# Performance work log

Hardware: AMD Instinct MI355X
Metric: run time of the kernel (lower is better)

The kernel has to match this reference:

```python
import jax, jax.numpy as jnp
import numpy as np
from jax import lax

# Stacked SimpleRNN (Keras): h_t = tanh(x_t @ W + h_{t-1} @ U + b).
# Dropout(0.5) is only active in training mode; this reference implements
# inference (training=None -> dropout disabled), matching model(x).

B, T, F = 512, 512, 78
HIDDENS = (16, 32, 64, 70)
NUM_CLASSES = 5


def _glorot(key, shape):
    fan_in, fan_out = shape[0], shape[1]
    lim = float(np.sqrt(6.0 / (fan_in + fan_out)))
    return jax.random.uniform(key, shape, jnp.float32, -lim, lim)


def setup_inputs() -> dict:
    key = jax.random.key(0)
    ks = jax.random.split(key, 16)
    x = jax.random.normal(ks[0], (B, T, F), jnp.float32)
    params = {}
    in_dim = F
    for i, h in enumerate(HIDDENS):
        params[f"W{i}"] = _glorot(ks[1 + 3 * i], (in_dim, h))
        params[f"U{i}"] = _glorot(ks[2 + 3 * i], (h, h))
        params[f"b{i}"] = jnp.zeros((h,), jnp.float32)
        in_dim = h
    params["Wd"] = _glorot(ks[13], (HIDDENS[-1], NUM_CLASSES))
    params["bd"] = jnp.zeros((NUM_CLASSES,), jnp.float32)
    return {"x": x, **params}


def _simple_rnn(x, W, U, b, return_sequences):
    # Precompute input projection for all timesteps: [B, T, H]
    xw = jnp.einsum("btf,fh->bth", x, W) + b
    h0 = jnp.zeros((x.shape[0], W.shape[1]), x.dtype)

    def step(h, xw_t):
        h_new = jnp.tanh(xw_t + h @ U)
        return h_new, h_new

    h_last, hs = lax.scan(step, h0, jnp.swapaxes(xw, 0, 1))  # scan over time
    if return_sequences:
        return jnp.swapaxes(hs, 0, 1)  # [B, T, H]
    return h_last  # [B, H]


def reference(x, W0, U0, b0, W1, U1, b1, W2, U2, b2, W3, U3, b3, Wd, bd):
    h = _simple_rnn(x, W0, U0, b0, True)
    h = _simple_rnn(h, W1, U1, b1, True)
    h = _simple_rnn(h, W2, U2, b2, True)
    h = _simple_rnn(h, W3, U3, b3, False)  # [B, 70]
    logits = h @ Wd + bd  # [B, 5]
    return jax.nn.softmax(logits, axis=-1)
```

## Files before the change

kernel.cpp:

```cpp
#include <hip/hip_runtime.h>
#include <cstddef>
#include <cstdint>

#define REC_ATTR __attribute__((amdgpu_waves_per_eu(1, 1)))

#define BB 512
#define TT 512
#define M_TOTAL (BB * TT)

#define LDS_BARRIER() asm volatile("s_waitcnt lgkmcnt(0)\n\ts_barrier" ::: "memory")

__device__ __forceinline__ float tanh_fast(float x) {
  float ax = fabsf(x);
  float e = __expf(ax + ax);
  float r = 1.0f - 2.0f / (e + 1.0f);
  return (x >= 0.0f) ? r : -r;
}

__device__ __forceinline__ void fma4(float4& a, float s, const float4 w) {
  a.x = fmaf(s, w.x, a.x);
  a.y = fmaf(s, w.y, a.y);
  a.z = fmaf(s, w.z, a.z);
  a.w = fmaf(s, w.w, a.w);
}

template<int K, int N, int CG>
__global__ __launch_bounds__(256)
void proj_kernel(const float* __restrict__ in, const float* __restrict__ W,
                 const float* __restrict__ bias, float* __restrict__ out, int M)
{
  constexpr int NP = CG * 4;
  constexpr int RG = 256 / CG;
  __shared__ __align__(16) float wlds[K][NP];
  __shared__ __align__(16) float blds[NP];
  const int tid = threadIdx.x;
  for (int idx = tid; idx < K * NP; idx += 256) {
    int k = idx / NP, jj = idx - k * NP;
    wlds[k][jj] = (jj < N) ? W[k * N + jj] : 0.0f;
  }
  if (tid < NP) blds[tid] = (tid < N) ? bias[tid] : 0.0f;
  __syncthreads();

  const int c = tid % CG;
  const int rg = tid / CG;
  if (rg >= RG) return;
  const int j0 = c * 4;
  const long row0 = (long)blockIdx.x * (RG * 4) + (long)rg * 4;

  float4 b4 = *reinterpret_cast<const float4*>(&blds[j0]);
  float4 acc[4] = {b4, b4, b4, b4};
  const float* inp[4];
  bool rv[4];
  #pragma unroll
  for (int rr = 0; rr < 4; ++rr) {
    long rowi = row0 + rr;
    rv[rr] = rowi < M;
    inp[rr] = in + (rv[rr] ? rowi : 0) * (long)K;
  }

  int k = 0;
  for (; k + 4 <= K; k += 4) {
    float4 w0 = *reinterpret_cast<const float4*>(&wlds[k + 0][j0]);
    float4 w1 = *reinterpret_cast<const float4*>(&wlds[k + 1][j0]);
    float4 w2 = *reinterpret_cast<const float4*>(&wlds[k + 2][j0]);
    float4 w3 = *reinterpret_cast<const float4*>(&wlds[k + 3][j0]);
    #pragma unroll
    for (int rr = 0; rr < 4; ++rr) {
      float2 i0 = *reinterpret_cast<const float2*>(inp[rr] + k);
      float2 i1 = *reinterpret_cast<const float2*>(inp[rr] + k + 2);
      fma4(acc[rr], i0.x, w0);
      fma4(acc[rr], i0.y, w1);
      fma4(acc[rr], i1.x, w2);
      fma4(acc[rr], i1.y, w3);
    }
  }
  for (; k < K; ++k) {
    float4 w0 = *reinterpret_cast<const float4*>(&wlds[k][j0]);
    #pragma unroll
    for (int rr = 0; rr < 4; ++rr) fma4(acc[rr], inp[rr][k], w0);
  }

  #pragma unroll
  for (int rr = 0; rr < 4; ++rr) {
    if (!rv[rr]) continue;
    long obase = (row0 + rr) * (long)N + j0;
    if constexpr ((N % 4) == 0) {
      *reinterpret_cast<float4*>(&out[obase]) = acc[rr];
    } else {
      if (j0 + 4 <= N) {
        *reinterpret_cast<float2*>(&out[obase]) = make_float2(acc[rr].x, acc[rr].y);
        *reinterpret_cast<float2*>(&out[obase + 2]) = make_float2(acc[rr].z, acc[rr].w);
      } else {
        float v[4] = {acc[rr].x, acc[rr].y, acc[rr].z, acc[rr].w};
        #pragma unroll
        for (int jj = 0; jj < 4; ++jj)
          if (j0 + jj < N) out[obase + jj] = v[jj];
      }
    }
  }
}

__global__ __launch_bounds__(64) REC_ATTR
void fused_rec16(const float* __restrict__ xw, const float* __restrict__ U,
                 const float* __restrict__ Wn, const float* __restrict__ bn,
                 float* __restrict__ xwn)
{
  constexpr int H = 16, ROWS = 4, HN = 32, CH = 16, NCH = TT / CH;
  constexpr int XINR = 264;
  const int tid = threadIdx.x;
  const int r = tid >> 4, j = tid & 15;
  const int c = tid & 31, pr = tid >> 5;
  __shared__ __align__(16) float xin[2][ROWS * XINR];
  __shared__ __align__(16) float xout[ROWS * CH * HN];
  __shared__ __align__(16) float hlds[ROWS][H];

  float u[H], w[H];
  #pragma unroll
  for (int kk = 0; kk < H; ++kk) {
    u[kk] = U[kk * H + j];
    w[kk] = Wn[kk * HN + c];
    asm volatile("" : "+v"(u[kk]), "+v"(w[kk]));
  }
  const float bc = bn[c];

  const int row0 = blockIdx.x * ROWS;
  const float* gin[ROWS];
  float* gout[ROWS];
  #pragma unroll
  for (int rr = 0; rr < ROWS; ++rr) {
    gin[rr] = xw + ((size_t)(row0 + rr) * TT) * H;
    gout[rr] = xwn + ((size_t)(row0 + rr) * TT) * HN;
  }
  for (int i = tid; i < ROWS * H; i += 64) reinterpret_cast<float*>(hlds)[i] = 0.0f;
  #pragma unroll
  for (int rr = 0; rr < ROWS; ++rr) {
    float4 v = reinterpret_cast<const float4*>(gin[rr])[tid];
    *reinterpret_cast<float4*>(&xin[0][rr * XINR + tid * 4]) = v;
  }

  for (int ch = 0; ch < NCH; ++ch) {
    const int buf = ch & 1, nb = buf ^ 1;
    const int ch1 = (ch + 1 < NCH) ? ch + 1 : ch;
    float4 nv[ROWS];
    #pragma unroll
    for (int rr = 0; rr < ROWS; ++rr)
      nv[rr] = reinterpret_cast<const float4*>(gin[rr] + (size_t)ch1 * CH * H)[tid];

    #pragma unroll
    for (int s = 0; s < CH; ++s) {
      float xv = xin[buf][r * XINR + s * H + j];
      float a0 = xv, a1 = 0.0f, a2 = 0.0f, a3 = 0.0f;
      const float* hb = &hlds[r][0];
      #pragma unroll
      for (int k4 = 0; k4 < H / 4; ++k4) {
        float4 h4 = *reinterpret_cast<const float4*>(hb + 4 * k4);
        a0 = fmaf(h4.x, u[4 * k4 + 0], a0);
        a1 = fmaf(h4.y, u[4 * k4 + 1], a1);
        a2 = fmaf(h4.z, u[4 * k4 + 2], a2);
        a3 = fmaf(h4.w, u[4 * k4 + 3], a3);
      }
      float hn = tanh_fast((a0 + a1) + (a2 + a3));
      hlds[r][j] = hn;
      const float* h0b = &hlds[2 * pr + 0][0];
      const float* h1b = &hlds[2 * pr + 1][0];
      float s0 = bc, s1 = bc, s2 = 0.0f, s3 = 0.0f;
      #pragma unroll
      for (int k4 = 0; k4 < H / 4; ++k4) {
        float4 ha = *reinterpret_cast<const float4*>(h0b + 4 * k4);
        float4 hc = *reinterpret_cast<const float4*>(h1b + 4 * k4);
        s0 = fmaf(ha.x, w[4 * k4 + 0], s0);
        s2 = fmaf(ha.y, w[4 * k4 + 1], s2);
        s0 = fmaf(ha.z, w[4 * k4 + 2], s0);
        s2 = fmaf(ha.w, w[4 * k4 + 3], s2);
        s1 = fmaf(hc.x, w[4 * k4 + 0], s1);
        s3 = fmaf(hc.y, w[4 * k4 + 1], s3);
        s1 = fmaf(hc.z, w[4 * k4 + 2], s1);
        s3 = fmaf(hc.w, w[4 * k4 + 3], s3);
      }
      xout[(2 * pr + 0) * (CH * HN) + s * HN + c] = s0 + s2;
      xout[(2 * pr + 1) * (CH * HN) + s * HN + c] = s1 + s3;
    }
    #pragma unroll
    for (int rr = 0; rr < ROWS; ++rr) {
      float* gslab = gout[rr] + (size_t)(ch * CH) * HN;
      #pragma unroll
      for (int q = 0; q < 2; ++q) {
        float4 f = reinterpret_cast<const float4*>(&xout[rr * (CH * HN)])[q * 64 + tid];
        reinterpret_cast<float4*>(gslab)[q * 64 + tid] = f;
      }
    }
    #pragma unroll
    for (int rr = 0; rr < ROWS; ++rr)
      *reinterpret_cast<float4*>(&xin[nb][rr * XINR + tid * 4]) = nv[rr];
  }
}

__global__ __launch_bounds__(64) REC_ATTR
void fused_rec32(const float* __restrict__ xw, const float* __restrict__ U,
                 const float* __restrict__ Wn, const float* __restrict__ bn,
                 float* __restrict__ xwn)
{
  constexpr int H = 32, ROWS = 2, HN = 64, CH = 16, NCH = TT / CH;
  constexpr int XINR = 520;
  const int tid = threadIdx.x;
  const int r = tid >> 5, j = tid & 31;
  const int c = tid;
  __shared__ __align__(16) float xin[2][ROWS * XINR];
  __shared__ __align__(16) float xout[ROWS * CH * HN];
  __shared__ __align__(16) float hlds[ROWS][H];

  float u[H], w[H];
  #pragma unroll
  for (int kk = 0; kk < H; ++kk) {
    u[kk] = U[kk * H + j];
    w[kk] = Wn[kk * HN + c];
    asm volatile("" : "+v"(u[kk]), "+v"(w[kk]));
  }
  const float bc = bn[c];

  const int row0 = blockIdx.x * ROWS;
  const float* gin[ROWS];
  float* gout[ROWS];
  #pragma unroll
  for (int rr = 0; rr < ROWS; ++rr) {
    gin[rr] = xw + ((size_t)(row0 + rr) * TT) * H;
    gout[rr] = xwn + ((size_t)(row0 + rr) * TT) * HN;
  }
  for (int i = tid; i < ROWS * H; i += 64) reinterpret_cast<float*>(hlds)[i] = 0.0f;
  #pragma unroll
  for (int rr = 0; rr < ROWS; ++rr)
    #pragma unroll
    for (int q = 0; q < 2; ++q) {
      float4 v = reinterpret_cast<const float4*>(gin[rr])[q * 64 + tid];
      *reinterpret_cast<float4*>(&xin[0][rr * XINR + (q * 64 + tid) * 4]) = v;
    }

  for (int ch = 0; ch < NCH; ++ch) {
    const int buf = ch & 1, nb = buf ^ 1;
    const int ch1 = (ch + 1 < NCH) ? ch + 1 : ch;
    float4 nv[ROWS][2];
    #pragma unroll
    for (int rr = 0; rr < ROWS; ++rr)
      #pragma unroll
      for (int q = 0; q < 2; ++q)
        nv[rr][q] = reinterpret_cast<const float4*>(gin[rr] + (size_t)ch1 * CH * H)[q * 64 + tid];

    #pragma unroll
    for (int s = 0; s < CH; ++s) {
      float xv = xin[buf][r * XINR + s * H + j];
      float a0 = xv, a1 = 0.0f, a2 = 0.0f, a3 = 0.0f;
      const float* hb = &hlds[r][0];
      #pragma unroll
      for (int k4 = 0; k4 < H / 4; ++k4) {
        float4 h4 = *reinterpret_cast<const float4*>(hb + 4 * k4);
        a0 = fmaf(h4.x, u[4 * k4 + 0], a0);
        a1 = fmaf(h4.y, u[4 * k4 + 1], a1);
        a2 = fmaf(h4.z, u[4 * k4 + 2], a2);
        a3 = fmaf(h4.w, u[4 * k4 + 3], a3);
      }
      float hn = tanh_fast((a0 + a1) + (a2 + a3));
      hlds[r][j] = hn;
      const float* h0b = &hlds[0][0];
      const float* h1b = &hlds[1][0];
      float s0 = bc, s1 = bc, s2 = 0.0f, s3 = 0.0f;
      #pragma unroll
      for (int k4 = 0; k4 < H / 4; ++k4) {
        float4 ha = *reinterpret_cast<const float4*>(h0b + 4 * k4);
        float4 hc = *reinterpret_cast<const float4*>(h1b + 4 * k4);
        s0 = fmaf(ha.x, w[4 * k4 + 0], s0);
        s2 = fmaf(ha.y, w[4 * k4 + 1], s2);
        s0 = fmaf(ha.z, w[4 * k4 + 2], s0);
        s2 = fmaf(ha.w, w[4 * k4 + 3], s2);
        s1 = fmaf(hc.x, w[4 * k4 + 0], s1);
        s3 = fmaf(hc.y, w[4 * k4 + 1], s3);
        s1 = fmaf(hc.z, w[4 * k4 + 2], s1);
        s3 = fmaf(hc.w, w[4 * k4 + 3], s3);
      }
      xout[0 * (CH * HN) + s * HN + c] = s0 + s2;
      xout[1 * (CH * HN) + s * HN + c] = s1 + s3;
    }
    #pragma unroll
    for (int rr = 0; rr < ROWS; ++rr) {
      float* gslab = gout[rr] + (size_t)(ch * CH) * HN;
      #pragma unroll
      for (int q = 0; q < 4; ++q) {
        float4 f = reinterpret_cast<const float4*>(&xout[rr * (CH * HN)])[q * 64 + tid];
        reinterpret_cast<float4*>(gslab)[q * 64 + tid] = f;
      }
    }
    #pragma unroll
    for (int rr = 0; rr < ROWS; ++rr)
      #pragma unroll
      for (int q = 0; q < 2; ++q)
        *reinterpret_cast<float4*>(&xin[nb][rr * XINR + (q * 64 + tid) * 4]) = nv[rr][q];
  }
}

__global__ __launch_bounds__(64) REC_ATTR
void rec64_kernel(const float* __restrict__ xw, const float* __restrict__ U,
                  float* __restrict__ hseq)
{
  constexpr int H = 64, CH = 16, NCH = TT / CH;
  const int tid = threadIdx.x;
  const int row = blockIdx.x;
  __shared__ __align__(16) float xin[2][CH * H];
  __shared__ __align__(16) float xout[CH * H];
  __shared__ __align__(16) float hlds[H];

  float u[H];
  #pragma unroll
  for (int kk = 0; kk < H; ++kk) {
    u[kk] = U[kk * H + tid];
    asm volatile("" : "+v"(u[kk]));
  }
  const float* gin = xw + ((size_t)row * TT) * H;
  float* gout = hseq + ((size_t)row * TT) * H;

  hlds[tid] = 0.0f;
  #pragma unroll
  for (int q = 0; q < 4; ++q) {
    float4 v = reinterpret_cast<const float4*>(gin)[q * 64 + tid];
    *reinterpret_cast<float4*>(&xin[0][(q * 64 + tid) * 4]) = v;
  }

  for (int ch = 0; ch < NCH; ++ch) {
    const int buf = ch & 1, nb = buf ^ 1;
    const int ch1 = (ch + 1 < NCH) ? ch + 1 : ch;
    float4 nv[4];
    #pragma unroll
    for (int q = 0; q < 4; ++q)
      nv[q] = reinterpret_cast<const float4*>(gin + (size_t)ch1 * CH * H)[q * 64 + tid];

    #pragma unroll
    for (int s = 0; s < CH; ++s) {
      float xv = xin[buf][s * H + tid];
      float a0 = xv, a1 = 0.0f, a2 = 0.0f, a3 = 0.0f;
      #pragma unroll
      for (int k4 = 0; k4 < H / 4; ++k4) {
        float4 h4 = *reinterpret_cast<const float4*>(&hlds[4 * k4]);
        a0 = fmaf(h4.x, u[4 * k4 + 0], a0);
        a1 = fmaf(h4.y, u[4 * k4 + 1], a1);
        a2 = fmaf(h4.z, u[4 * k4 + 2], a2);
        a3 = fmaf(h4.w, u[4 * k4 + 3], a3);
      }
      float hn = tanh_fast((a0 + a1) + (a2 + a3));
      hlds[tid] = hn;
      xout[s * H + tid] = hn;
    }
    float* gslab = gout + (size_t)(ch * CH) * H;
    #pragma unroll
    for (int q = 0; q < 4; ++q) {
      float4 f = reinterpret_cast<const float4*>(xout)[q * 64 + tid];
      reinterpret_cast<float4*>(gslab)[q * 64 + tid] = f;
    }
    #pragma unroll
    for (int q = 0; q < 4; ++q)
      *reinterpret_cast<float4*>(&xin[nb][(q * 64 + tid) * 4]) = nv[q];
  }
}

__global__ __launch_bounds__(128) REC_ATTR
void rec70_kernel(const float* __restrict__ xw, const float* __restrict__ U,
                  const float* __restrict__ Wd, const float* __restrict__ bd,
                  float* __restrict__ outp)
{
  constexpr int H = 70, HP = 72, CH = 16, NCH = TT / CH, SLAB = CH * H;
  constexpr int NL = 9;
  const int tid = threadIdx.x;
  const int row = blockIdx.x;
  const bool act = tid < H;
  const int j = act ? tid : 0;

  __shared__ __align__(16) float xin[2][1152];
  __shared__ __align__(16) float hbuf[2][HP];

  float u[HP];
  #pragma unroll
  for (int kk = 0; kk < HP; ++kk) {
    u[kk] = (kk < H && act) ? U[kk * H + j] : 0.0f;
    asm volatile("" : "+v"(u[kk]));
  }

  const float* gin = xw + ((size_t)row * TT) * H;
  for (int i = tid; i < 2 * HP; i += 128) reinterpret_cast<float*>(hbuf)[i] = 0.0f;
  #pragma unroll
  for (int q = 0; q < NL; ++q) {
    int idx = q * 128 + tid;
    xin[0][idx] = (idx < SLAB) ? gin[idx] : 0.0f;
  }
  __syncthreads();

  for (int ch = 0; ch < NCH; ++ch) {
    const int buf = ch & 1, nb = buf ^ 1;
    const int ch1 = (ch + 1 < NCH) ? ch + 1 : ch;
    const float* gslab = gin + (size_t)ch1 * SLAB;
    float nv[NL];
    #pragma unroll
    for (int q = 0; q < NL; ++q) {
      int idx = q * 128 + tid;
      nv[q] = (idx < SLAB) ? gslab[idx] : 0.0f;
    }

    #pragma unroll
    for (int s = 0; s < CH; ++s) {
      float xv = xin[buf][s * H + j];
      const float* hb = &hbuf[s & 1][0];
      float a0 = xv, a1 = 0.0f, a2 = 0.0f, a3 = 0.0f;
      #pragma unroll
      for (int k4 = 0; k4 < HP / 4; ++k4) {
        float4 h4 = *reinterpret_cast<const float4*>(hb + 4 * k4);
        a0 = fmaf(h4.x, u[4 * k4 + 0], a0);
        a1 = fmaf(h4.y, u[4 * k4 + 1], a1);
        a2 = fmaf(h4.z, u[4 * k4 + 2], a2);
        a3 = fmaf(h4.w, u[4 * k4 + 3], a3);
      }
      float hn = tanh_fast((a0 + a1) + (a2 + a3));
      if (act) hbuf[(s & 1) ^ 1][j] = hn;
      if (s == CH - 1) {
        #pragma unroll
        for (int q = 0; q < NL; ++q) xin[nb][q * 128 + tid] = nv[q];
      }
      LDS_BARRIER();
    }
  }

  float l = 0.0f;
  if (tid < 5) {
    l = bd[tid];
    #pragma unroll
    for (int kk = 0; kk < H; ++kk)
      l = fmaf(hbuf[0][kk], Wd[kk * 5 + tid], l);
  }
  float l0 = __shfl(l, 0), l1 = __shfl(l, 1), l2 = __shfl(l, 2),
        l3 = __shfl(l, 3), l4 = __shfl(l, 4);
  float m = fmaxf(fmaxf(fmaxf(l0, l1), fmaxf(l2, l3)), l4);
  float s = __expf(l0 - m) + __expf(l1 - m) + __expf(l2 - m) +
            __expf(l3 - m) + __expf(l4 - m);
  if (tid < 5)
    outp[(size_t)row * 5 + tid] = __expf(l - m) / s;
}

extern "C" void kernel_launch(void* const* d_in, const int* in_sizes, int n_in,
                              void* d_out, int out_size, void* d_ws, size_t ws_size,
                              hipStream_t stream)
{
  const float* x  = (const float*)d_in[0];
  const float* W0 = (const float*)d_in[1];
  const float* U0 = (const float*)d_in[2];
  const float* b0 = (const float*)d_in[3];
  const float* W1 = (const float*)d_in[4];
  const float* U1 = (const float*)d_in[5];
  const float* b1 = (const float*)d_in[6];
  const float* W2 = (const float*)d_in[7];
  const float* U2 = (const float*)d_in[8];
  const float* b2 = (const float*)d_in[9];
  const float* W3 = (const float*)d_in[10];
  const float* U3 = (const float*)d_in[11];
  const float* b3 = (const float*)d_in[12];
  const float* Wd = (const float*)d_in[13];
  const float* bd = (const float*)d_in[14];
  float* outp = (float*)d_out;

  float* A  = (float*)d_ws;
  float* Bv = (float*)((char*)d_ws + 73400320);

  const int M = M_TOTAL;

  proj_kernel<78, 16, 4><<<M / 256, 256, 0, stream>>>(x, W0, b0, A, M);
  fused_rec16<<<BB / 4, 64, 0, stream>>>(A, U0, W1, b1, Bv);
  fused_rec32<<<BB / 2, 64, 0, stream>>>(Bv, U1, W2, b2, A);
  rec64_kernel<<<BB, 64, 0, stream>>>(A, U2, Bv);
  proj_kernel<64, 70, 18><<<(M + 55) / 56, 256, 0, stream>>>(Bv, W3, b3, A, M);
  rec70_kernel<<<BB, 128, 0, stream>>>(A, U3, Wd, bd, outp);
}
```

Before: 979.9 us.

## Process two batch rows per block in rec64 and rec70 recurrences

The H=64 and H=70 recurrence kernels now advance two independent batch rows per block, sharing the register-resident U matrix and interleaving the two FMA chains. This halves the grid to 256 blocks and gives each wave two independent dependency chains, hiding LDS and FMA latency in the serial time loop. The softmax epilogue is split so each wave handles one row. The cost is more registers and LDS per block and fewer blocks, which may leave part of the GPU's compute units idle.

After: 1.647 ms. +68.1%, slower.

```diff
diff --git a/kernel.cpp b/kernel.cpp
--- a/kernel.cpp
+++ b/kernel.cpp
@@ -302,10 +302,10 @@
 {
   constexpr int H = 64, CH = 16, NCH = TT / CH;
   const int tid = threadIdx.x;
-  const int row = blockIdx.x;
-  __shared__ __align__(16) float xin[2][CH * H];
-  __shared__ __align__(16) float xout[CH * H];
-  __shared__ __align__(16) float hlds[H];
+  const int rowA = blockIdx.x * 2, rowB = rowA + 1;
+  __shared__ __align__(16) float xinA[2][CH * H], xinB[2][CH * H];
+  __shared__ __align__(16) float xoutA[CH * H], xoutB[CH * H];
+  __shared__ __align__(16) float hA[H], hB[H];
 
   float u[H];
   #pragma unroll
@@ -313,49 +313,75 @@
     u[kk] = U[kk * H + tid];
     asm volatile("" : "+v"(u[kk]));
   }
-  const float* gin = xw + ((size_t)row * TT) * H;
-  float* gout = hseq + ((size_t)row * TT) * H;
-
-  hlds[tid] = 0.0f;
+  const float* ginA = xw + ((size_t)rowA * TT) * H;
+  const float* ginB = xw + ((size_t)rowB * TT) * H;
+  float* goutA = hseq + ((size_t)rowA * TT) * H;
+  float* goutB = hseq + ((size_t)rowB * TT) * H;
+
+  hA[tid] = 0.0f;
+  hB[tid] = 0.0f;
   #pragma unroll
   for (int q = 0; q < 4; ++q) {
-    float4 v = reinterpret_cast<const float4*>(gin)[q * 64 + tid];
-    *reinterpret_cast<float4*>(&xin[0][(q * 64 + tid) * 4]) = v;
+    *reinterpret_cast<float4*>(&xinA[0][(q * 64 + tid) * 4]) =
+        reinterpret_cast<const float4*>(ginA)[q * 64 + tid];
+    *reinterpret_cast<float4*>(&xinB[0][(q * 64 + tid) * 4]) =
+        reinterpret_cast<const float4*>(ginB)[q * 64 + tid];
   }
 
   for (int ch = 0; ch < NCH; ++ch) {
     const int buf = ch & 1, nb = buf ^ 1;
     const int ch1 = (ch + 1 < NCH) ? ch + 1 : ch;
-    float4 nv[4];
-    #pragma unroll
-    for (int q = 0; q < 4; ++q)
-      nv[q] = reinterpret_cast<const float4*>(gin + (size_t)ch1 * CH * H)[q * 64 + tid];
-
+    float4 nvA[4], nvB[4];
+    #pragma unroll
+    for (int q = 0; q < 4; ++q) {
+      nvA[q] = reinterpret_cast<const float4*>(ginA + (size_t)ch1 * CH * H)[q * 64 + tid];
+      nvB[q] = reinterpret_cast<const float4*>(ginB + (size_t)ch1 * CH * H)[q * 64 + tid];
+    }
+    float xvA[CH], xvB[CH];
     #pragma unroll
     for (int s = 0; s < CH; ++s) {
-      float xv = xin[buf][s * H + tid];
-      float a0 = xv, a1 = 0.0f, a2 = 0.0f, a3 = 0.0f;
+      xvA[s] = xinA[buf][s * H + tid];
+      xvB[s] = xinB[buf][s * H + tid];
+    }
+
+    #pragma unroll
+    for (int s = 0; s < CH; ++s) {
+      float a0 = xvA[s], a1 = 0.0f, a2 = 0.0f, a3 = 0.0f;
+      float b0 = xvB[s], b1 = 0.0f, b2 = 0.0f, b3 = 0.0f;
       #pragma unroll
       for (int k4 = 0; k4 < H / 4; ++k4) {
-        float4 h4 = *reinterpret_cast<const float4*>(&hlds[4 * k4]);
-        a0 = fmaf(h4.x, u[4 * k4 + 0], a0);
-        a1 = fmaf(h4.y, u[4 * k4 + 1], a1);
-        a2 = fmaf(h4.z, u[4 * k4 + 2], a2);
-        a3 = fmaf(h4.w, u[4 * k4 + 3], a3);
-      }
-      float hn = tanh_fast((a0 + a1) + (a2 + a3));
-      hlds[tid] = hn;
-      xout[s * H + tid] = hn;
-    }
-    float* gslab = gout + (size_t)(ch * CH) * H;
+        float4 h4a = *reinterpret_cast<const float4*>(&hA[4 * k4]);
+        float4 h4b = *reinterpret_cast<const float4*>(&hB[4 * k4]);
+        a0 = fmaf(h4a.x, u[4 * k4 + 0], a0);
+        a1 = fmaf(h4a.y, u[4 * k4 + 1], a1);
+        a2 = fmaf(h4a.z, u[4 * k4 + 2], a2);
+        a3 = fmaf(h4a.w, u[4 * k4 + 3], a3);
+        b0 = fmaf(h4b.x, u[4 * k4 + 0], b0);
+        b1 = fmaf(h4b.y, u[4 * k4 + 1], b1);
+        b2 = fmaf(h4b.z, u[4 * k4 + 2], b2);
+        b3 = fmaf(h4b.w, u[4 * k4 + 3], b3);
+      }
+      float hnA = tanh_fast((a0 + a1) + (a2 + a3));
+      float hnB = tanh_fast((b0 + b1) + (b2 + b3));
+      hA[tid] = hnA;
+      hB[tid] = hnB;
+      xoutA[s * H + tid] = hnA;
+      xoutB[s * H + tid] = hnB;
+    }
+    float* gsA = goutA + (size_t)(ch * CH) * H;
+    float* gsB = goutB + (size_t)(ch * CH) * H;
     #pragma unroll
     for (int q = 0; q < 4; ++q) {
-      float4 f = reinterpret_cast<const float4*>(xout)[q * 64 + tid];
-      reinterpret_cast<float4*>(gslab)[q * 64 + tid] = f;
-    }
-    #pragma unroll
-    for (int q = 0; q < 4; ++q)
-      *reinterpret_cast<float4*>(&xin[nb][(q * 64 + tid) * 4]) = nv[q];
+      reinterpret_cast<float4*>(gsA)[q * 64 + tid] =
+          reinterpret_cast<const float4*>(xoutA)[q * 64 + tid];
+      reinterpret_cast<float4*>(gsB)[q * 64 + tid] =
+          reinterpret_cast<const float4*>(xoutB)[q * 64 + tid];
+    }
+    #pragma unroll
+    for (int q = 0; q < 4; ++q) {
+      *reinterpret_cast<float4*>(&xinA[nb][(q * 64 + tid) * 4]) = nvA[q];
+      *reinterpret_cast<float4*>(&xinB[nb][(q * 64 + tid) * 4]) = nvB[q];
+    }
   }
 }
 
@@ -367,12 +393,12 @@
   constexpr int H = 70, HP = 72, CH = 16, NCH = TT / CH, SLAB = CH * H;
   constexpr int NL = 9;
   const int tid = threadIdx.x;
-  const int row = blockIdx.x;
+  const int rowA = blockIdx.x * 2;
   const bool act = tid < H;
   const int j = act ? tid : 0;
 
-  __shared__ __align__(16) float xin[2][1152];
-  __shared__ __align__(16) float hbuf[2][HP];
+  __shared__ __align__(16) float xinA[2][1152], xinB[2][1152];
+  __shared__ __align__(16) float hbufA[2][HP], hbufB[2][HP];
 
   float u[HP];
   #pragma unroll
@@ -381,63 +407,89 @@
     asm volatile("" : "+v"(u[kk]));
   }
 
-  const float* gin = xw + ((size_t)row * TT) * H;
-  for (int i = tid; i < 2 * HP; i += 128) reinterpret_cast<float*>(hbuf)[i] = 0.0f;
+  const float* ginA = xw + ((size_t)rowA * TT) * H;
+  const float* ginB = xw + ((size_t)(rowA + 1) * TT) * H;
+  for (int i = tid; i < 2 * HP; i += 128) {
+    reinterpret_cast<float*>(hbufA)[i] = 0.0f;
+    reinterpret_cast<float*>(hbufB)[i] = 0.0f;
+  }
   #pragma unroll
   for (int q = 0; q < NL; ++q) {
     int idx = q * 128 + tid;
-    xin[0][idx] = (idx < SLAB) ? gin[idx] : 0.0f;
+    xinA[0][idx] = (idx < SLAB) ? ginA[idx] : 0.0f;
+    xinB[0][idx] = (idx < SLAB) ? ginB[idx] : 0.0f;
   }
   __syncthreads();
 
   for (int ch = 0; ch < NCH; ++ch) {
     const int buf = ch & 1, nb = buf ^ 1;
     const int ch1 = (ch + 1 < NCH) ? ch + 1 : ch;
-    const float* gslab = gin + (size_t)ch1 * SLAB;
-    float nv[NL];
+    float nvA[NL], nvB[NL];
     #pragma unroll
     for (int q = 0; q < NL; ++q) {
       int idx = q * 128 + tid;
-      nv[q] = (idx < SLAB) ? gslab[idx] : 0.0f;
-    }
-
+      nvA[q] = (idx < SLAB) ? (ginA + (size_t)ch1 * SLAB)[idx] : 0.0f;
+      nvB[q] = (idx < SLAB) ? (ginB + (size_t)ch1 * SLAB)[idx] : 0.0f;
+    }
+    float xvA[CH], xvB[CH];
     #pragma unroll
     for (int s = 0; s < CH; ++s) {
-      float xv = xin[buf][s * H + j];
-      const float* hb = &hbuf[s & 1][0];
-      float a0 = xv, a1 = 0.0f, a2 = 0.0f, a3 = 0.0f;
+      xvA[s] = xinA[buf][s * H + j];
+      xvB[s] = xinB[buf][s * H + j];
+    }
+
+    #pragma unroll
+    for (int s = 0; s < CH; ++s) {
+      const float* hbA = &hbufA[s & 1][0];
+      const float* hbB = &hbufB[s & 1][0];
+      float a0 = xvA[s], a1 = 0.0f, a2 = 0.0f, a3 = 0.0f;
+      float b0 = xvB[s], b1 = 0.0f, b2 = 0.0f, b3 = 0.0f;
       #pragma unroll
       for (int k4 = 0; k4 < HP / 4; ++k4) {
-        float4 h4 = *reinterpret_cast<const float4*>(hb + 4 * k4);
-        a0 = fmaf(h4.x, u[4 * k4 + 0], a0);
-        a1 = fmaf(h4.y, u[4 * k4 + 1], a1);
-        a2 = fmaf(h4.z, u[4 * k4 + 2], a2);
-        a3 = fmaf(h4.w, u[4 * k4 + 3], a3);
-      }
-      float hn = tanh_fast((a0 + a1) + (a2 + a3));
-      if (act) hbuf[(s & 1) ^ 1][j] = hn;
+        float4 h4a = *reinterpret_cast<const float4*>(hbA + 4 * k4);
+        float4 h4b = *reinterpret_cast<const float4*>(hbB + 4 * k4);
+        a0 = fmaf(h4a.x, u[4 * k4 + 0], a0);
+        a1 = fmaf(h4a.y, u[4 * k4 + 1], a1);
+        a2 = fmaf(h4a.z, u[4 * k4 + 2], a2);
+        a3 = fmaf(h4a.w, u[4 * k4 + 3], a3);
+        b0 = fmaf(h4b.x, u[4 * k4 + 0], b0);
+        b1 = fmaf(h4b.y, u[4 * k4 + 1], b1);
+        b2 = fmaf(h4b.z, u[4 * k4 + 2], b2);
+        b3 = fmaf(h4b.w, u[4 * k4 + 3], b3);
+      }
+      float hnA = tanh_fast((a0 + a1) + (a2 + a3));
+      float hnB = tanh_fast((b0 + b1) + (b2 + b3));
+      if (act) {
+        hbufA[(s & 1) ^ 1][j] = hnA;
+        hbufB[(s & 1) ^ 1][j] = hnB;
+      }
       if (s == CH - 1) {
         #pragma unroll
-        for (int q = 0; q < NL; ++q) xin[nb][q * 128 + tid] = nv[q];
+        for (int q = 0; q < NL; ++q) {
+          xinA[nb][q * 128 + tid] = nvA[q];
+          xinB[nb][q * 128 + tid] = nvB[q];
+        }
       }
       LDS_BARRIER();
     }
   }
 
+  const int wv = tid >> 6, lane = tid & 63;
+  const float* hb = wv ? &hbufB[0][0] : &hbufA[0][0];
   float l = 0.0f;
-  if (tid < 5) {
-    l = bd[tid];
+  if (lane < 5) {
+    l = bd[lane];
     #pragma unroll
     for (int kk = 0; kk < H; ++kk)
-      l = fmaf(hbuf[0][kk], Wd[kk * 5 + tid], l);
+      l = fmaf(hb[kk], Wd[kk * 5 + lane], l);
   }
   float l0 = __shfl(l, 0), l1 = __shfl(l, 1), l2 = __shfl(l, 2),
         l3 = __shfl(l, 3), l4 = __shfl(l, 4);
   float m = fmaxf(fmaxf(fmaxf(l0, l1), fmaxf(l2, l3)), l4);
   float s = __expf(l0 - m) + __expf(l1 - m) + __expf(l2 - m) +
             __expf(l3 - m) + __expf(l4 - m);
-  if (tid < 5)
-    outp[(size_t)row * 5 + tid] = __expf(l - m) / s;
+  if (lane < 5)
+    outp[(size_t)(rowA + wv) * 5 + lane] = __expf(l - m) / s;
 }
 
 extern "C" void kernel_launch(void* const* d_in, const int* in_sizes, int n_in,
@@ -469,7 +521,7 @@
   proj_kernel<78, 16, 4><<<M / 256, 256, 0, stream>>>(x, W0, b0, A, M);
   fused_rec16<<<BB / 4, 64, 0, stream>>>(A, U0, W1, b1, Bv);
   fused_rec32<<<BB / 2, 64, 0, stream>>>(Bv, U1, W2, b2, A);
-  rec64_kernel<<<BB, 64, 0, stream>>>(A, U2, Bv);
+  rec64_kernel<<<BB / 2, 64, 0, stream>>>(A, U2, Bv);
   proj_kernel<64, 70, 18><<<(M + 55) / 56, 256, 0, stream>>>(Bv, W3, b3, A, M);
-  rec70_kernel<<<BB, 128, 0, stream>>>(A, U3, Wd, bd, outp);
-}
+  rec70_kernel<<<BB / 2, 128, 0, stream>>>(A, U3, Wd, bd, outp);
+}
```
